# Kernel optimization log

Hardware: AMD Instinct MI355X
Metric: run time of the kernel (lower is better)

## Reference

```python
import jax, jax.numpy as jnp
import numpy as np

K_NEIGHBORS = 3


def setup_inputs() -> dict:
    key = jax.random.key(0)
    k1, k2 = jax.random.split(key)
    B, E, Hl, Wl = 8, 768, 32, 32   # ViT-Base latent grid for 512x512 / patch 16
    N = 20000                        # size of fitted kNN memory bank
    embeddings = jax.random.normal(k1, (B, E, Hl, Wl), dtype=jnp.float32)
    bank = jax.random.normal(k2, (N, E), dtype=jnp.float32)
    return {"embeddings": embeddings, "bank": bank, "out_size": 512}


def reference(embeddings, bank, out_size):
    # embeddings: [B, E, Hl, Wl]; bank: [N, E]
    B, E, Hl, Wl = embeddings.shape
    # permute(0,2,3,1) then flatten H,W -> queries [B, Hl*Wl, E]
    q = jnp.transpose(embeddings, (0, 2, 3, 1)).reshape(B, Hl * Wl, E)
    # squared Euclidean distances via ||q||^2 + ||b||^2 - 2 q.b
    q2 = jnp.sum(q * q, axis=-1, keepdims=True)            # [B, Q, 1]
    b2 = jnp.sum(bank * bank, axis=-1)                      # [N]
    d2 = q2 + b2[None, None, :] - 2.0 * jnp.einsum('bqe,ne->bqn', q, bank)  # [B, Q, N]
    # k nearest = top-k of negated squared distance
    neg_top, _ = jax.lax.top_k(-d2, K_NEIGHBORS)            # [B, Q, K]
    dist = jnp.sqrt(jnp.maximum(-neg_top, 1e-12))           # Euclidean distances
    scores = dist.mean(axis=-1).reshape(B, Hl, Wl)          # mean over k neighbors
    # F.interpolate(..., mode='bilinear') default align_corners=False == half-pixel
    out = jax.image.resize(scores[:, None, :, :], (B, 1, out_size, out_size), method='bilinear')
    return out
```

## Files before the change

kernel.cpp:

```cpp
#include <hip/hip_runtime.h>
#include <math.h>

#define KD     768
#define MT     128
#define NT     128
#define KB     128
#define NKC    6
#define NSPLIT 32
#define BIGF   3.0e38f

typedef __attribute__((ext_vector_type(4))) int   i32x4;
typedef __attribute__((ext_vector_type(8))) int   i32x8;
typedef __attribute__((ext_vector_type(4))) float f32x4;

__device__ __forceinline__ unsigned f2e4m3(float x) {
    unsigned u = __float_as_uint(x);
    unsigned s = (u >> 24) & 0x80u;
    float ax = __uint_as_float(u & 0x7fffffffu);
    if (ax < 0.015625f) {
        int n = (int)rintf(ax * 512.0f);
        if (n >= 8) return s | 0x08u;
        return s | (unsigned)n;
    }
    if (ax >= 464.0f) return s | 0x7Eu;
    unsigned m = __float_as_uint(ax);
    unsigned low = m & 0xFFFFFu;
    unsigned r = m >> 20;
    r += (low > 0x80000u) || (low == 0x80000u && (r & 1u));
    int ef = (int)(r >> 3) - 120;
    return s | ((unsigned)ef << 3) | (r & 7u);
}

__device__ __forceinline__ void ins3(float* t, float v) {
    float lo0 = fminf(t[0], v);
    float hi0 = fmaxf(t[0], v);
    float lo1 = fminf(t[1], hi0);
    float hi1 = fmaxf(t[1], hi0);
    float lo2 = fminf(t[2], hi1);
    t[0] = lo0; t[1] = lo1; t[2] = lo2;
}
__device__ __forceinline__ void async16(unsigned char* lds, const unsigned char* g) {
    __builtin_amdgcn_global_load_lds(
        (const __attribute__((address_space(1))) unsigned int*)g,
        (__attribute__((address_space(3))) unsigned int*)lds, 16, 0, 0);
}

__global__ void q_prep_k(const float* __restrict__ emb, unsigned char* __restrict__ qf8,
                         float* __restrict__ q2) {
    __shared__ float s[64][65];
    int bx  = blockIdx.x;
    int b   = bx / 48;
    int rem = bx % 48;
    int hw0 = (rem & 15) * 64;
    int eg  = rem >> 4;
    const float* src = emb + (size_t)b * KD * 1024;
    unsigned int* q4 = (unsigned int*)qf8;
    float part[4] = {0.f, 0.f, 0.f, 0.f};
    for (int e0 = eg * 256; e0 < eg * 256 + 256; e0 += 64) {
        __syncthreads();
        #pragma unroll
        for (int i = 0; i < 16; ++i) {
            int idx = threadIdx.x + i * 256;
            int ee = idx >> 6, hh = idx & 63;
            s[ee][hh] = src[(size_t)(e0 + ee) * 1024 + hw0 + hh];
        }
        __syncthreads();
        #pragma unroll
        for (int i = 0; i < 4; ++i) {
            int slot = threadIdx.x + i * 256;
            int qq = slot >> 4, e4 = slot & 15;
            float v0 = s[e4 * 4 + 0][qq], v1 = s[e4 * 4 + 1][qq];
            float v2 = s[e4 * 4 + 2][qq], v3 = s[e4 * 4 + 3][qq];
            unsigned p = f2e4m3(v0) | (f2e4m3(v1) << 8)
                       | (f2e4m3(v2) << 16) | (f2e4m3(v3) << 24);
            q4[((size_t)b * 1024 + hw0 + qq) * (KD / 4) + e0 / 4 + e4] = p;
            part[i] = fmaf(v0, v0, part[i]); part[i] = fmaf(v1, v1, part[i]);
            part[i] = fmaf(v2, v2, part[i]); part[i] = fmaf(v3, v3, part[i]);
        }
    }
    #pragma unroll
    for (int i = 0; i < 4; ++i) {
        float p = part[i];
        #pragma unroll
        for (int off = 1; off < 16; off <<= 1) p += __shfl_xor(p, off, 64);
        if ((threadIdx.x & 15) == 0) {
            int qq = (threadIdx.x + i * 256) >> 4;
            atomicAdd(&q2[b * 1024 + hw0 + qq], p);
        }
    }
}

__global__ void bank_prep_k(const float* __restrict__ bank, unsigned char* __restrict__ bf8,
                            float* __restrict__ b2, int N, int Npad) {
    int gid = blockIdx.x * 256 + threadIdx.x;
    int row = gid >> 6, lane = gid & 63;
    if (row >= Npad) return;
    unsigned int* b4 = (unsigned int*)bf8;
    if (row < N) {
        const float4* src = (const float4*)(bank + (size_t)row * KD);
        float s = 0.f;
        #pragma unroll
        for (int i = 0; i < KD / 256; ++i) {
            float4 v = src[lane + i * 64];
            s = fmaf(v.x, v.x, s); s = fmaf(v.y, v.y, s);
            s = fmaf(v.z, v.z, s); s = fmaf(v.w, v.w, s);
            unsigned p = f2e4m3(v.x) | (f2e4m3(v.y) << 8)
                       | (f2e4m3(v.z) << 16) | (f2e4m3(v.w) << 24);
            b4[(size_t)row * (KD / 4) + lane + i * 64] = p;
        }
        #pragma unroll
        for (int off = 32; off; off >>= 1) s += __shfl_down(s, off, 64);
        if (lane == 0) b2[row] = s;
    } else {
        #pragma unroll
        for (int i = 0; i < KD / 256; ++i) b4[(size_t)row * (KD / 4) + lane + i * 64] = 0;
        if (lane == 0) b2[row] = BIGF;
    }
}

__device__ __forceinline__ void stage_pair(unsigned char (*stage)[MT * KB],
                                           const unsigned char* gA, const unsigned char* gB,
                                           int k0, int tid) {
    #pragma unroll
    for (int h = 0; h < 2; ++h) {
        #pragma unroll
        for (int i = 0; i < 2; ++i) {
            int s = tid + i * 512;
            int m = s >> 3, g = s & 7;
            int G = g ^ (m & 7);
            async16(&stage[2 * h + 0][s * 16], gA + (size_t)m * KD + k0 + h * KB + G * 16);
        }
        #pragma unroll
        for (int i = 0; i < 2; ++i) {
            int s = tid + i * 512;
            int m = s >> 3, g = s & 7;
            int G = g ^ (m & 7);
            async16(&stage[2 * h + 1][s * 16], gB + (size_t)m * KD + k0 + h * KB + G * 16);
        }
    }
}

__device__ __forceinline__ i32x8 frag_read(const unsigned char* st, int base, int o0, int o1) {
    i32x4 lo = *(const i32x4*)&st[base + o0];
    i32x4 hi = *(const i32x4*)&st[base + o1];
    return __builtin_shufflevector(lo, hi, 0, 1, 2, 3, 4, 5, 6, 7);
}

__device__ __forceinline__ void mfma_chunk(const unsigned char* stA, const unsigned char* stB,
                                           f32x4 acc[2][4], int wm, int wn,
                                           int l15, int quad, int xr) {
    const int o0 = ((2 * quad) ^ xr) * 16;
    const int o1 = ((2 * quad + 1) ^ xr) * 16;
    i32x8 af[2];
    #pragma unroll
    for (int mi = 0; mi < 2; ++mi)
        af[mi] = frag_read(stA, (32 * wm + 16 * mi + l15) * KB, o0, o1);
    #pragma unroll
    for (int ni = 0; ni < 4; ++ni) {
        i32x8 bfr = frag_read(stB, (64 * wn + 16 * ni + l15) * KB, o0, o1);
        #pragma unroll
        for (int mi = 0; mi < 2; ++mi)
            acc[mi][ni] = __builtin_amdgcn_mfma_scale_f32_16x16x128_f8f6f4(
                af[mi], bfr, acc[mi][ni], 0, 0,
                0, 127, 0, 127);
    }
}

__device__ __forceinline__ void do_epilogue(const f32x4 acc[2][4], const float b2v[4],
                                            float* top3) {
    #pragma unroll
    for (int ni = 0; ni < 4; ++ni)
        #pragma unroll
        for (int mi = 0; mi < 2; ++mi)
            #pragma unroll
            for (int r = 0; r < 4; ++r) {
                float s = fmaf(-2.0f, acc[mi][ni][r], b2v[ni]);
                ins3(&top3[(mi * 4 + r) * 3], s);
            }
}

__global__ __launch_bounds__(512, 4)
void knn_mfma_k(const unsigned char* __restrict__ qf8, const unsigned char* __restrict__ bf8,
                const float* __restrict__ b2g, float* __restrict__ cand,
                int ntiles, int Q) {
    __shared__ unsigned char stage[4][MT * KB];

    const int tid  = threadIdx.x;
    const int lane = tid & 63;
    const int quad = lane >> 4;
    const int l15  = lane & 15;
    const int wid  = tid >> 6;
    const int wm   = wid & 3;
    const int wn   = wid >> 2;
    const int xr   = l15 & 7;

    const int bx   = blockIdx.x;
    const int xcd  = bx & 7;
    const int rr_  = bx >> 9;
    const int jj   = (bx >> 3) & 63;
    const int mt   = (xcd & 3) * 16 + (jj & 15);
    const int sp   = (jj >> 4) + 4 * (xcd >> 2) + 8 * rr_;
    const int Mbase = mt * MT;

    float top3[24];
    #pragma unroll
    for (int i = 0; i < 24; ++i) top3[i] = BIGF;

    const unsigned char* gA = qf8 + (size_t)Mbase * KD;

    f32x4 acc[2][4];
    float b2v[4];
    bool first = true;

    for (int nt = sp; nt < ntiles; nt += NSPLIT) {
        const size_t nbase = (size_t)nt * NT;
        const unsigned char* gB = bf8 + nbase * KD;

        __syncthreads();
        stage_pair(stage, gA, gB, 0, tid);
        float t0 = b2g[nbase + 64 * wn + 0  + l15];
        float t1 = b2g[nbase + 64 * wn + 16 + l15];
        float t2 = b2g[nbase + 64 * wn + 32 + l15];
        float t3 = b2g[nbase + 64 * wn + 48 + l15];
        if (!first) do_epilogue(acc, b2v, top3);
        first = false;
        b2v[0] = t0; b2v[1] = t1; b2v[2] = t2; b2v[3] = t3;
        #pragma unroll
        for (int a = 0; a < 2; ++a)
            #pragma unroll
            for (int b = 0; b < 4; ++b) acc[a][b] = (f32x4){0.f, 0.f, 0.f, 0.f};
        __syncthreads();
        mfma_chunk(stage[0], stage[1], acc, wm, wn, l15, quad, xr);
        mfma_chunk(stage[2], stage[3], acc, wm, wn, l15, quad, xr);

        #pragma unroll
        for (int p = 1; p < NKC / 2; ++p) {
            __syncthreads();
            stage_pair(stage, gA, gB, 2 * p * KB, tid);
            __syncthreads();
            mfma_chunk(stage[0], stage[1], acc, wm, wn, l15, quad, xr);
            mfma_chunk(stage[2], stage[3], acc, wm, wn, l15, quad, xr);
        }
    }
    do_epilogue(acc, b2v, top3);

    #pragma unroll
    for (int mi = 0; mi < 2; ++mi)
        #pragma unroll
        for (int r = 0; r < 4; ++r) {
            float a0 = top3[(mi * 4 + r) * 3 + 0];
            float a1 = top3[(mi * 4 + r) * 3 + 1];
            float a2 = top3[(mi * 4 + r) * 3 + 2];
            #pragma unroll
            for (int off = 1; off < 16; off <<= 1) {
                float b0 = __shfl_xor(a0, off, 64);
                float b1 = __shfl_xor(a1, off, 64);
                float b2x = __shfl_xor(a2, off, 64);
                float t[3] = {a0, a1, a2};
                ins3(t, b0); ins3(t, b1); ins3(t, b2x);
                a0 = t[0]; a1 = t[1]; a2 = t[2];
            }
            if (l15 == 0) {
                int row = Mbase + 32 * wm + 16 * mi + 4 * quad + r;
                float* o = cand + ((size_t)(sp * 2 + wn) * Q + row) * 3;
                o[0] = a0; o[1] = a1; o[2] = a2;
            }
        }
}

__global__ void scores_k(const float* __restrict__ cand, const float* __restrict__ q2g,
                         float* __restrict__ scores, int Q) {
    int gid  = blockIdx.x * 256 + threadIdx.x;
    int q    = gid >> 6;
    int lane = gid & 63;
    if (q >= Q) return;
    const float* c = cand + ((size_t)lane * Q + q) * 3;
    float a0 = c[0], a1 = c[1], a2 = c[2];
    #pragma unroll
    for (int off = 1; off < 64; off <<= 1) {
        float b0 = __shfl_xor(a0, off, 64);
        float b1 = __shfl_xor(a1, off, 64);
        float b2x = __shfl_xor(a2, off, 64);
        float t[3] = {a0, a1, a2};
        ins3(t, b0); ins3(t, b1); ins3(t, b2x);
        a0 = t[0]; a1 = t[1]; a2 = t[2];
    }
    if (lane == 0) {
        float q2 = q2g[q];
        float s = (sqrtf(fmaxf(q2 + a0, 1e-12f)) +
                   sqrtf(fmaxf(q2 + a1, 1e-12f)) +
                   sqrtf(fmaxf(q2 + a2, 1e-12f))) * (1.f / 3.f);
        scores[q] = s;
    }
}

__global__ void upsample_k(const float* __restrict__ scores, float* __restrict__ out, int total) {
    int idx = blockIdx.x * blockDim.x + threadIdx.x;
    if (idx >= total) return;
    int x = idx & 511;
    int y = (idx >> 9) & 511;
    int b = idx >> 18;
    float sx = (x + 0.5f) * (1.f / 16.f) - 0.5f;
    float sy = (y + 0.5f) * (1.f / 16.f) - 0.5f;
    int x0 = (int)floorf(sx);
    int y0 = (int)floorf(sy);
    float wx = sx - (float)x0;
    float wy = sy - (float)y0;
    int x0c = min(max(x0, 0), 31), x1c = min(max(x0 + 1, 0), 31);
    int y0c = min(max(y0, 0), 31), y1c = min(max(y0 + 1, 0), 31);
    const float* sb = scores + (size_t)b * 1024;
    float v00 = sb[y0c * 32 + x0c], v01 = sb[y0c * 32 + x1c];
    float v10 = sb[y1c * 32 + x0c], v11 = sb[y1c * 32 + x1c];
    float v0 = v00 + wx * (v01 - v00);
    float v1 = v10 + wx * (v11 - v10);
    out[idx] = v0 + wy * (v1 - v0);
}

extern "C" void kernel_launch(void* const* d_in, const int* in_sizes, int n_in,
                              void* d_out, int out_size, void* d_ws, size_t ws_size,
                              hipStream_t stream) {
    const float* emb  = (const float*)d_in[0];
    const float* bank = (const float*)d_in[1];
    const int Q      = in_sizes[0] / KD;
    const int B      = Q / 1024;
    const int Nbank  = in_sizes[1] / KD;
    const int ntiles = (Nbank + NT - 1) / NT;
    const int Npad   = ntiles * NT;
    const int Mtiles = Q / MT;

    unsigned char* qf8 = (unsigned char*)d_ws;
    unsigned char* bf8 = qf8 + (size_t)Q * KD;
    float* fbase  = (float*)(bf8 + (size_t)Npad * KD);
    float* q2     = fbase;
    float* b2     = q2 + Q;
    float* cand   = b2 + Npad;
    float* scores = cand + (size_t)NSPLIT * 2 * Q * 3;
    float* out    = (float*)d_out;

    hipMemsetAsync(q2, 0, Q * sizeof(float), stream);
    hipLaunchKernelGGL(q_prep_k, dim3(B * 48), dim3(256), 0, stream, emb, qf8, q2);
    hipLaunchKernelGGL(bank_prep_k, dim3((Npad * 64 + 255) / 256), dim3(256), 0, stream,
                       bank, bf8, b2, Nbank, Npad);
    hipLaunchKernelGGL(knn_mfma_k, dim3(Mtiles * NSPLIT), dim3(512), 0, stream,
                       qf8, bf8, b2, cand, ntiles, Q);
    hipLaunchKernelGGL(scores_k, dim3((Q * 64 + 255) / 256), dim3(256), 0, stream,
                       cand, q2, scores, Q);
    hipLaunchKernelGGL(upsample_k, dim3((out_size + 255) / 256), dim3(256), 0, stream,
                       scores, out, out_size);
}
```

Before: 380.4 us.

## Enlarge kNN GEMM tiles to 256x256 with double-buffered async K-chunk pipeline

Raises the block tile from 128x128 to 256x256, so each wave now holds a 4x8 MFMA accumulator grid, and cuts the N-split from 32 to 8. A 64KB double-buffered LDS pipeline prefetches the next K chunk while MFMAs run on the current one. The b2 norms are preloaded into shared memory, and the scores reduction shrinks to 16 partials. The aim is more operand reuse per byte staged and fewer full barriers, at the cost of higher register and LDS pressure (occupancy 2), fewer blocks (256), and more padding rows in the bank.

Result: slower. 583.2 us (+53.3%).

```diff
diff --git a/kernel.cpp b/kernel.cpp
--- a/kernel.cpp
+++ b/kernel.cpp
@@ -2,11 +2,11 @@
 #include <math.h>
 
 #define KD     768
-#define MT     128
-#define NT     128
+#define BM     256
+#define BN     256
 #define KB     128
 #define NKC    6
-#define NSPLIT 32
+#define NSPLIT 8
 #define BIGF   3.0e38f
 
 typedef __attribute__((ext_vector_type(4))) int   i32x4;
@@ -118,25 +118,22 @@
     }
 }
 
-__device__ __forceinline__ void stage_pair(unsigned char (*stage)[MT * KB],
-                                           const unsigned char* gA, const unsigned char* gB,
-                                           int k0, int tid) {
-    #pragma unroll
-    for (int h = 0; h < 2; ++h) {
-        #pragma unroll
-        for (int i = 0; i < 2; ++i) {
-            int s = tid + i * 512;
-            int m = s >> 3, g = s & 7;
-            int G = g ^ (m & 7);
-            async16(&stage[2 * h + 0][s * 16], gA + (size_t)m * KD + k0 + h * KB + G * 16);
-        }
-        #pragma unroll
-        for (int i = 0; i < 2; ++i) {
-            int s = tid + i * 512;
-            int m = s >> 3, g = s & 7;
-            int G = g ^ (m & 7);
-            async16(&stage[2 * h + 1][s * 16], gB + (size_t)m * KD + k0 + h * KB + G * 16);
-        }
+__device__ __forceinline__ void stage_chunk(unsigned char* buf,
+                                            const unsigned char* gA, const unsigned char* gB,
+                                            int k0, int tid) {
+    #pragma unroll
+    for (int i = 0; i < 4; ++i) {
+        int s = tid + i * 512;
+        int m = s >> 3, g = s & 7;
+        int G = g ^ (m & 7);
+        async16(buf + s * 16, gA + (size_t)m * KD + k0 + G * 16);
+    }
+    #pragma unroll
+    for (int i = 0; i < 4; ++i) {
+        int s = tid + i * 512;
+        int m = s >> 3, g = s & 7;
+        int G = g ^ (m & 7);
+        async16(buf + 32768 + s * 16, gB + (size_t)m * KD + k0 + G * 16);
     }
 }
 
@@ -147,43 +144,46 @@
 }
 
 __device__ __forceinline__ void mfma_chunk(const unsigned char* stA, const unsigned char* stB,
-                                           f32x4 acc[2][4], int wm, int wn,
+                                           f32x4 acc[4][8], int wm, int wn,
                                            int l15, int quad, int xr) {
     const int o0 = ((2 * quad) ^ xr) * 16;
     const int o1 = ((2 * quad + 1) ^ xr) * 16;
-    i32x8 af[2];
-    #pragma unroll
-    for (int mi = 0; mi < 2; ++mi)
-        af[mi] = frag_read(stA, (32 * wm + 16 * mi + l15) * KB, o0, o1);
-    #pragma unroll
-    for (int ni = 0; ni < 4; ++ni) {
-        i32x8 bfr = frag_read(stB, (64 * wn + 16 * ni + l15) * KB, o0, o1);
-        #pragma unroll
-        for (int mi = 0; mi < 2; ++mi)
+    i32x8 af[4];
+    #pragma unroll
+    for (int mi = 0; mi < 4; ++mi)
+        af[mi] = frag_read(stA, (64 * wm + 16 * mi + l15) * KB, o0, o1);
+    #pragma unroll
+    for (int ni = 0; ni < 8; ++ni) {
+        i32x8 bfr = frag_read(stB, (128 * wn + 16 * ni + l15) * KB, o0, o1);
+        #pragma unroll
+        for (int mi = 0; mi < 4; ++mi)
             acc[mi][ni] = __builtin_amdgcn_mfma_scale_f32_16x16x128_f8f6f4(
                 af[mi], bfr, acc[mi][ni], 0, 0,
                 0, 127, 0, 127);
     }
 }
 
-__device__ __forceinline__ void do_epilogue(const f32x4 acc[2][4], const float b2v[4],
-                                            float* top3) {
-    #pragma unroll
-    for (int ni = 0; ni < 4; ++ni)
-        #pragma unroll
-        for (int mi = 0; mi < 2; ++mi)
+__device__ __forceinline__ void do_epilogue(const f32x4 acc[4][8], const float* b2p,
+                                            int l15, float* top3) {
+    #pragma unroll
+    for (int ni = 0; ni < 8; ++ni) {
+        float b2v = b2p[16 * ni + l15];
+        #pragma unroll
+        for (int mi = 0; mi < 4; ++mi)
             #pragma unroll
             for (int r = 0; r < 4; ++r) {
-                float s = fmaf(-2.0f, acc[mi][ni][r], b2v[ni]);
+                float s = fmaf(-2.0f, acc[mi][ni][r], b2v);
                 ins3(&top3[(mi * 4 + r) * 3], s);
             }
-}
-
-__global__ __launch_bounds__(512, 4)
+    }
+}
+
+__global__ __launch_bounds__(512, 2)
 void knn_mfma_k(const unsigned char* __restrict__ qf8, const unsigned char* __restrict__ bf8,
                 const float* __restrict__ b2g, float* __restrict__ cand,
                 int ntiles, int Q) {
-    __shared__ unsigned char stage[4][MT * KB];
+    __shared__ unsigned char stage[2][65536];
+    __shared__ float b2s[12 * 256];
 
     const int tid  = threadIdx.x;
     const int lane = tid & 63;
@@ -196,56 +196,60 @@
 
     const int bx   = blockIdx.x;
     const int xcd  = bx & 7;
-    const int rr_  = bx >> 9;
-    const int jj   = (bx >> 3) & 63;
-    const int mt   = (xcd & 3) * 16 + (jj & 15);
-    const int sp   = (jj >> 4) + 4 * (xcd >> 2) + 8 * rr_;
-    const int Mbase = mt * MT;
-
-    float top3[24];
-    #pragma unroll
-    for (int i = 0; i < 24; ++i) top3[i] = BIGF;
-
+    const int j    = bx >> 3;
+    const int mt   = xcd * 4 + (j & 3);
+    const int sp   = j >> 2;
+    const int Mbase = mt * BM;
+
+    const int numnt = (ntiles - sp + NSPLIT - 1) / NSPLIT;
+
+    for (int i = tid; i < numnt * 256; i += 512) {
+        int slot = i >> 8, col = i & 255;
+        int nt = sp + slot * NSPLIT;
+        b2s[i] = b2g[(size_t)nt * BN + col];
+    }
     const unsigned char* gA = qf8 + (size_t)Mbase * KD;
 
-    f32x4 acc[2][4];
-    float b2v[4];
-    bool first = true;
-
-    for (int nt = sp; nt < ntiles; nt += NSPLIT) {
-        const size_t nbase = (size_t)nt * NT;
-        const unsigned char* gB = bf8 + nbase * KD;
-
-        __syncthreads();
-        stage_pair(stage, gA, gB, 0, tid);
-        float t0 = b2g[nbase + 64 * wn + 0  + l15];
-        float t1 = b2g[nbase + 64 * wn + 16 + l15];
-        float t2 = b2g[nbase + 64 * wn + 32 + l15];
-        float t3 = b2g[nbase + 64 * wn + 48 + l15];
-        if (!first) do_epilogue(acc, b2v, top3);
-        first = false;
-        b2v[0] = t0; b2v[1] = t1; b2v[2] = t2; b2v[3] = t3;
-        #pragma unroll
-        for (int a = 0; a < 2; ++a)
-            #pragma unroll
-            for (int b = 0; b < 4; ++b) acc[a][b] = (f32x4){0.f, 0.f, 0.f, 0.f};
-        __syncthreads();
-        mfma_chunk(stage[0], stage[1], acc, wm, wn, l15, quad, xr);
-        mfma_chunk(stage[2], stage[3], acc, wm, wn, l15, quad, xr);
-
-        #pragma unroll
-        for (int p = 1; p < NKC / 2; ++p) {
-            __syncthreads();
-            stage_pair(stage, gA, gB, 2 * p * KB, tid);
-            __syncthreads();
-            mfma_chunk(stage[0], stage[1], acc, wm, wn, l15, quad, xr);
-            mfma_chunk(stage[2], stage[3], acc, wm, wn, l15, quad, xr);
-        }
-    }
-    do_epilogue(acc, b2v, top3);
-
-    #pragma unroll
-    for (int mi = 0; mi < 2; ++mi)
+    float top3[48];
+    #pragma unroll
+    for (int i = 0; i < 48; ++i) top3[i] = BIGF;
+    f32x4 acc[4][8];
+    #pragma unroll
+    for (int a = 0; a < 4; ++a)
+        #pragma unroll
+        for (int b = 0; b < 8; ++b) acc[a][b] = (f32x4){0.f, 0.f, 0.f, 0.f};
+
+    asm volatile("s_waitcnt vmcnt(0) lgkmcnt(0)" ::: "memory");
+    __syncthreads();
+
+    stage_chunk(stage[0], gA, bf8 + (size_t)sp * BN * KD, 0, tid);
+
+    int cur = 0;
+    for (int i = 0; i < numnt; ++i) {
+        const int inext = (i + 1 < numnt) ? i + 1 : i;
+        const unsigned char* gBc = bf8 + (size_t)(sp + i     * NSPLIT) * BN * KD;
+        const unsigned char* gBn = bf8 + (size_t)(sp + inext * NSPLIT) * BN * KD;
+        #pragma unroll
+        for (int kc = 0; kc < NKC; ++kc) {
+            asm volatile("s_waitcnt vmcnt(0)" ::: "memory");
+            __builtin_amdgcn_s_barrier();
+            if (kc < NKC - 1) stage_chunk(stage[cur ^ 1], gA, gBc, (kc + 1) * KB, tid);
+            else              stage_chunk(stage[cur ^ 1], gA, gBn, 0, tid);
+            if (kc == 0 && i > 0) {
+                do_epilogue(acc, &b2s[(i - 1) * 256 + 128 * wn], l15, top3);
+                #pragma unroll
+                for (int a = 0; a < 4; ++a)
+                    #pragma unroll
+                    for (int b = 0; b < 8; ++b) acc[a][b] = (f32x4){0.f, 0.f, 0.f, 0.f};
+            }
+            mfma_chunk(stage[cur], stage[cur] + 32768, acc, wm, wn, l15, quad, xr);
+            cur ^= 1;
+        }
+    }
+    do_epilogue(acc, &b2s[(numnt - 1) * 256 + 128 * wn], l15, top3);
+
+    #pragma unroll
+    for (int mi = 0; mi < 4; ++mi)
         #pragma unroll
         for (int r = 0; r < 4; ++r) {
             float a0 = top3[(mi * 4 + r) * 3 + 0];
@@ -261,7 +265,7 @@
                 a0 = t[0]; a1 = t[1]; a2 = t[2];
             }
             if (l15 == 0) {
-                int row = Mbase + 32 * wm + 16 * mi + 4 * quad + r;
+                int row = Mbase + 64 * wm + 16 * mi + 4 * quad + r;
                 float* o = cand + ((size_t)(sp * 2 + wn) * Q + row) * 3;
                 o[0] = a0; o[1] = a1; o[2] = a2;
             }
@@ -271,13 +275,13 @@
 __global__ void scores_k(const float* __restrict__ cand, const float* __restrict__ q2g,
                          float* __restrict__ scores, int Q) {
     int gid  = blockIdx.x * 256 + threadIdx.x;
-    int q    = gid >> 6;
-    int lane = gid & 63;
+    int q    = gid >> 4;
+    int p    = gid & 15;
     if (q >= Q) return;
-    const float* c = cand + ((size_t)lane * Q + q) * 3;
+    const float* c = cand + ((size_t)p * Q + q) * 3;
     float a0 = c[0], a1 = c[1], a2 = c[2];
     #pragma unroll
-    for (int off = 1; off < 64; off <<= 1) {
+    for (int off = 1; off < 16; off <<= 1) {
         float b0 = __shfl_xor(a0, off, 64);
         float b1 = __shfl_xor(a1, off, 64);
         float b2x = __shfl_xor(a2, off, 64);
@@ -285,7 +289,7 @@
         ins3(t, b0); ins3(t, b1); ins3(t, b2x);
         a0 = t[0]; a1 = t[1]; a2 = t[2];
     }
-    if (lane == 0) {
+    if (p == 0) {
         float q2 = q2g[q];
         float s = (sqrtf(fmaxf(q2 + a0, 1e-12f)) +
                    sqrtf(fmaxf(q2 + a1, 1e-12f)) +
@@ -324,9 +328,9 @@
     const int Q      = in_sizes[0] / KD;
     const int B      = Q / 1024;
     const int Nbank  = in_sizes[1] / KD;
-    const int ntiles = (Nbank + NT - 1) / NT;
-    const int Npad   = ntiles * NT;
-    const int Mtiles = Q / MT;
+    const int ntiles = (Nbank + BN - 1) / BN;
+    const int Npad   = ntiles * BN;
+    const int Mtiles = Q / BM;
 
     unsigned char* qf8 = (unsigned char*)d_ws;
     unsigned char* bf8 = qf8 + (size_t)Q * KD;
@@ -343,7 +347,7 @@
                        bank, bf8, b2, Nbank, Npad);
     hipLaunchKernelGGL(knn_mfma_k, dim3(Mtiles * NSPLIT), dim3(512), 0, stream,
                        qf8, bf8, b2, cand, ntiles, Q);
-    hipLaunchKernelGGL(scores_k, dim3((Q * 64 + 255) / 256), dim3(256), 0, stream,
+    hipLaunchKernelGGL(scores_k, dim3((Q * 16 + 255) / 256), dim3(256), 0, stream,
                        cand, q2, scores, Q);
     hipLaunchKernelGGL(upsample_k, dim3((out_size + 255) / 256), dim3(256), 0, stream,
                        scores, out, out_size);
```

## Keep query fragments in registers and triple-buffer bank tiles with async prefetch

Applied to the files above, without the earlier changes.

The query A-fragments for the whole K dimension are loaded once into registers instead of being restaged through shared memory for every bank tile. Bank tiles are streamed through a 3-slot LDS ring with async loads issued two chunks ahead, synchronised by vmcnt waits and one barrier per chunk instead of two. Bank norms are preloaded into LDS. In exchange, register pressure rises a lot (launch bounds drop from 4 to 2 blocks per CU), which lowers occupancy.

New measurement: 378.9 us. About the same (-0.4%).

```diff
diff --git a/kernel.cpp b/kernel.cpp
--- a/kernel.cpp
+++ b/kernel.cpp
@@ -118,25 +118,14 @@
     }
 }
 
-__device__ __forceinline__ void stage_pair(unsigned char (*stage)[MT * KB],
-                                           const unsigned char* gA, const unsigned char* gB,
-                                           int k0, int tid) {
-    #pragma unroll
-    for (int h = 0; h < 2; ++h) {
-        #pragma unroll
-        for (int i = 0; i < 2; ++i) {
-            int s = tid + i * 512;
-            int m = s >> 3, g = s & 7;
-            int G = g ^ (m & 7);
-            async16(&stage[2 * h + 0][s * 16], gA + (size_t)m * KD + k0 + h * KB + G * 16);
-        }
-        #pragma unroll
-        for (int i = 0; i < 2; ++i) {
-            int s = tid + i * 512;
-            int m = s >> 3, g = s & 7;
-            int G = g ^ (m & 7);
-            async16(&stage[2 * h + 1][s * 16], gB + (size_t)m * KD + k0 + h * KB + G * 16);
-        }
+__device__ __forceinline__ void stage_b(unsigned char* buf, const unsigned char* gB,
+                                        int k0, int tid) {
+    #pragma unroll
+    for (int i = 0; i < 2; ++i) {
+        int s = tid + i * 512;
+        int m = s >> 3, g = s & 7;
+        int G = g ^ (m & 7);
+        async16(buf + s * 16, gB + (size_t)m * KD + k0 + G * 16);
     }
 }
 
@@ -146,44 +135,12 @@
     return __builtin_shufflevector(lo, hi, 0, 1, 2, 3, 4, 5, 6, 7);
 }
 
-__device__ __forceinline__ void mfma_chunk(const unsigned char* stA, const unsigned char* stB,
-                                           f32x4 acc[2][4], int wm, int wn,
-                                           int l15, int quad, int xr) {
-    const int o0 = ((2 * quad) ^ xr) * 16;
-    const int o1 = ((2 * quad + 1) ^ xr) * 16;
-    i32x8 af[2];
-    #pragma unroll
-    for (int mi = 0; mi < 2; ++mi)
-        af[mi] = frag_read(stA, (32 * wm + 16 * mi + l15) * KB, o0, o1);
-    #pragma unroll
-    for (int ni = 0; ni < 4; ++ni) {
-        i32x8 bfr = frag_read(stB, (64 * wn + 16 * ni + l15) * KB, o0, o1);
-        #pragma unroll
-        for (int mi = 0; mi < 2; ++mi)
-            acc[mi][ni] = __builtin_amdgcn_mfma_scale_f32_16x16x128_f8f6f4(
-                af[mi], bfr, acc[mi][ni], 0, 0,
-                0, 127, 0, 127);
-    }
-}
-
-__device__ __forceinline__ void do_epilogue(const f32x4 acc[2][4], const float b2v[4],
-                                            float* top3) {
-    #pragma unroll
-    for (int ni = 0; ni < 4; ++ni)
-        #pragma unroll
-        for (int mi = 0; mi < 2; ++mi)
-            #pragma unroll
-            for (int r = 0; r < 4; ++r) {
-                float s = fmaf(-2.0f, acc[mi][ni][r], b2v[ni]);
-                ins3(&top3[(mi * 4 + r) * 3], s);
-            }
-}
-
-__global__ __launch_bounds__(512, 4)
+__global__ __launch_bounds__(512, 2)
 void knn_mfma_k(const unsigned char* __restrict__ qf8, const unsigned char* __restrict__ bf8,
                 const float* __restrict__ b2g, float* __restrict__ cand,
                 int ntiles, int Q) {
-    __shared__ unsigned char stage[4][MT * KB];
+    __shared__ unsigned char bst[3][NT * KB];
+    __shared__ float b2s[5 * NT];
 
     const int tid  = threadIdx.x;
     const int lane = tid & 63;
@@ -202,47 +159,88 @@
     const int sp   = (jj >> 4) + 4 * (xcd >> 2) + 8 * rr_;
     const int Mbase = mt * MT;
 
+    const int numnt = (ntiles - sp + NSPLIT - 1) / NSPLIT;
+
+    for (int idx = tid; idx < numnt * NT; idx += 512) {
+        int slot = idx >> 7, col = idx & 127;
+        b2s[idx] = b2g[(size_t)(sp + slot * NSPLIT) * NT + col];
+    }
+
+    const unsigned char* gA = qf8 + ((size_t)Mbase + 32 * wm + l15) * KD + quad * 32;
+    i32x8 af[NKC][2];
+    #pragma unroll
+    for (int kc = 0; kc < NKC; ++kc)
+        #pragma unroll
+        for (int mi = 0; mi < 2; ++mi) {
+            const i32x4* p = (const i32x4*)(gA + (size_t)mi * 16 * KD + kc * KB);
+            i32x4 lo = p[0];
+            i32x4 hi = p[1];
+            af[kc][mi] = __builtin_shufflevector(lo, hi, 0, 1, 2, 3, 4, 5, 6, 7);
+        }
+
     float top3[24];
     #pragma unroll
     for (int i = 0; i < 24; ++i) top3[i] = BIGF;
-
-    const unsigned char* gA = qf8 + (size_t)Mbase * KD;
-
     f32x4 acc[2][4];
-    float b2v[4];
-    bool first = true;
-
-    for (int nt = sp; nt < ntiles; nt += NSPLIT) {
-        const size_t nbase = (size_t)nt * NT;
-        const unsigned char* gB = bf8 + nbase * KD;
-
-        __syncthreads();
-        stage_pair(stage, gA, gB, 0, tid);
-        float t0 = b2g[nbase + 64 * wn + 0  + l15];
-        float t1 = b2g[nbase + 64 * wn + 16 + l15];
-        float t2 = b2g[nbase + 64 * wn + 32 + l15];
-        float t3 = b2g[nbase + 64 * wn + 48 + l15];
-        if (!first) do_epilogue(acc, b2v, top3);
-        first = false;
-        b2v[0] = t0; b2v[1] = t1; b2v[2] = t2; b2v[3] = t3;
+    #pragma unroll
+    for (int a = 0; a < 2; ++a)
+        #pragma unroll
+        for (int b = 0; b < 4; ++b) acc[a][b] = (f32x4){0.f, 0.f, 0.f, 0.f};
+
+    const int o0 = ((2 * quad) ^ xr) * 16;
+    const int o1 = ((2 * quad + 1) ^ xr) * 16;
+    int bb[4];
+    #pragma unroll
+    for (int ni = 0; ni < 4; ++ni) bb[ni] = (64 * wn + 16 * ni + l15) * KB;
+
+    __syncthreads();
+
+    const unsigned char* gB0 = bf8 + (size_t)sp * NT * KD;
+    stage_b(bst[0], gB0, 0, tid);
+    stage_b(bst[1], gB0, KB, tid);
+
+    for (int i = 0; i < numnt; ++i) {
+        const unsigned char* gBc = bf8 + (size_t)(sp + i * NSPLIT) * NT * KD;
+        const bool last = (i == numnt - 1);
+        const unsigned char* gBn = last ? gBc
+                                 : bf8 + (size_t)(sp + (i + 1) * NSPLIT) * NT * KD;
+        #pragma unroll
+        for (int kc = 0; kc < NKC; ++kc) {
+            if (last && kc == NKC - 1) asm volatile("s_waitcnt vmcnt(0)" ::: "memory");
+            else                       asm volatile("s_waitcnt vmcnt(2)" ::: "memory");
+            __builtin_amdgcn_s_barrier();
+            if (!(last && kc >= NKC - 2)) {
+                if (kc < NKC - 2) stage_b(bst[(kc + 2) % 3], gBc, (kc + 2) * KB, tid);
+                else              stage_b(bst[(kc + 2) % 3], gBn, (kc - 4) * KB, tid);
+            }
+            const unsigned char* st = bst[kc % 3];
+            #pragma unroll
+            for (int ni = 0; ni < 4; ++ni) {
+                i32x8 bfr = frag_read(st, bb[ni], o0, o1);
+                #pragma unroll
+                for (int mi = 0; mi < 2; ++mi)
+                    acc[mi][ni] = __builtin_amdgcn_mfma_scale_f32_16x16x128_f8f6f4(
+                        af[kc][mi], bfr, acc[mi][ni], 0, 0,
+                        0, 127, 0, 127);
+            }
+        }
+        const float* b2p = &b2s[i * NT + 64 * wn];
+        #pragma unroll
+        for (int ni = 0; ni < 4; ++ni) {
+            float b2v = b2p[16 * ni + l15];
+            #pragma unroll
+            for (int mi = 0; mi < 2; ++mi)
+                #pragma unroll
+                for (int r = 0; r < 4; ++r) {
+                    float s = fmaf(-2.0f, acc[mi][ni][r], b2v);
+                    ins3(&top3[(mi * 4 + r) * 3], s);
+                }
+        }
         #pragma unroll
         for (int a = 0; a < 2; ++a)
             #pragma unroll
             for (int b = 0; b < 4; ++b) acc[a][b] = (f32x4){0.f, 0.f, 0.f, 0.f};
-        __syncthreads();
-        mfma_chunk(stage[0], stage[1], acc, wm, wn, l15, quad, xr);
-        mfma_chunk(stage[2], stage[3], acc, wm, wn, l15, quad, xr);
-
-        #pragma unroll
-        for (int p = 1; p < NKC / 2; ++p) {
-            __syncthreads();
-            stage_pair(stage, gA, gB, 2 * p * KB, tid);
-            __syncthreads();
-            mfma_chunk(stage[0], stage[1], acc, wm, wn, l15, quad, xr);
-            mfma_chunk(stage[2], stage[3], acc, wm, wn, l15, quad, xr);
-        }
-    }
-    do_epilogue(acc, b2v, top3);
+    }
 
     #pragma unroll
     for (int mi = 0; mi < 2; ++mi)
```
